# Kernel tuning notes

Hardware: AMD Instinct MI355X
Metric: run time of the kernel (lower is better)

The kernel has to match this reference:

```python
import jax, jax.numpy as jnp
import numpy as np

B, T, C = 4, 2048, 1024
H = 16
D = C // H  # head_size = 64


def setup_inputs() -> dict:
    key = jax.random.key(0)
    ks = jax.random.split(key, 9)
    s = 1.0 / np.sqrt(C).astype(np.float32)
    return {
        "x": jax.random.normal(ks[0], (B, T, C), dtype=jnp.float32),
        "Wq": jax.random.normal(ks[1], (C, C), dtype=jnp.float32) * s,
        "bq": jnp.zeros((C,), dtype=jnp.float32),
        "Wk": jax.random.normal(ks[2], (C, C), dtype=jnp.float32) * s,
        "bk": jnp.zeros((C,), dtype=jnp.float32),
        "Wv": jax.random.normal(ks[3], (C, C), dtype=jnp.float32) * s,
        "bv": jnp.zeros((C,), dtype=jnp.float32),
        "Wp": jax.random.normal(ks[4], (C, C), dtype=jnp.float32) * s,
        "bp": jnp.zeros((C,), dtype=jnp.float32),
    }


def reference(x, Wq, bq, Wk, bk, Wv, bv, Wp, bp):
    # Linear projections, then split heads: (B, T, C) -> (B, H, T, D)
    def heads(t):
        return t.reshape(B, T, H, D).transpose(0, 2, 1, 3)

    q = heads(x @ Wq + bq)
    k = heads(x @ Wk + bk)
    v = heads(x @ Wv + bv)

    scale = 1.0 / np.sqrt(D).astype(np.float32)
    att = jnp.einsum("bhqd,bhkd->bhqk", q, k) * scale  # (B, H, T, T)
    att = jax.nn.softmax(att, axis=-1)
    y = jnp.einsum("bhqk,bhkd->bhqd", att, v)  # (B, H, T, D)
    y = y.transpose(0, 2, 1, 3).reshape(B, T, C)
    return y @ Wp + bp
```

## Files before the change

kernel.cpp:

```cpp
#include <hip/hip_runtime.h>

typedef unsigned int uint;
typedef unsigned short ushort;

typedef __bf16 bf16x8 __attribute__((ext_vector_type(8)));
typedef __bf16 bf16x2 __attribute__((ext_vector_type(2)));
typedef float f32x4 __attribute__((ext_vector_type(4)));
typedef float f32x16 __attribute__((ext_vector_type(16)));
typedef uint uint2v __attribute__((ext_vector_type(2)));

union U4 { uint4 u; bf16x8 v; };
union UB2 { bf16x2 v; uint u; };

__device__ __forceinline__ ushort f2bf(float f){
  uint u = __float_as_uint(f);
  u += 0x7fffu + ((u >> 16) & 1u);
  return (ushort)(u >> 16);
}

__device__ __forceinline__ uint packbf(float lo, float hi){
  UB2 t; t.v[0] = (__bf16)lo; t.v[1] = (__bf16)hi;
  return t.u;
}

__device__ __forceinline__ float exp2a(float x){
  float r; asm("v_exp_f32 %0, %1" : "=v"(r) : "v"(x)); return r;
}

__device__ __forceinline__ void gload16(const void* g, void* l){
  __builtin_amdgcn_global_load_lds((const __attribute__((address_space(1))) uint*)g,
                                   (__attribute__((address_space(3))) uint*)l, 16, 0, 0);
}

__device__ __forceinline__ f32x16 mfma32(U4 a, U4 b, f32x16 c){
  return __builtin_amdgcn_mfma_f32_32x32x16_bf16(a.v, b.v, c, 0, 0, 0);
}

__global__ __launch_bounds__(256, 3) void gemm_qkv(
    const ushort* __restrict__ xh, const ushort* __restrict__ wbase,
    const float* __restrict__ bq, const float* __restrict__ bk,
    const float* __restrict__ bv,
    ushort* __restrict__ Qb, ushort* __restrict__ Kb, ushort* __restrict__ Vtb,
    float qscale)
{
  __shared__ uint4 smem4[2048];
  char* sAh = (char*)smem4;
  char* sBh = (char*)smem4 + 16384;

  const int tid  = threadIdx.x;
  const int lane = tid & 63;
  const int wid  = tid >> 6;
  const int wm = (wid >> 1) * 64;
  const int wn = (wid & 1) * 64;

  int hwlin = blockIdx.y * 64 + blockIdx.x;
  int xcd = hwlin & 7, io = hwlin >> 3;
  int mb  = xcd * 8 + (io & 7);
  int nv  = io >> 3;
  int nb  = nv & 7;
  int w   = nv >> 3;
  const long tm = (long)mb * 128;
  const long tn = (long)nb * 128;

  const char* gA = (const char*)xh;
  const char* gB = (const char*)(wbase + (long)w * 1048576);

  f32x4 acc[4][4] = {};

  for (int ks = 0; ks < 8; ks++){
    const int koff = ks * 128;
    #pragma unroll
    for (int c = 0; c < 4; c++){
      int o   = (tid + 256*c) * 16;
      int row = o >> 7;
      int src = (o & 127) ^ ((row & 7) << 4);
      gload16(gA + (tm + row)*2048 + koff + src, sAh + o);
      gload16(gB + (tn + row)*2048 + koff + src, sBh + o);
    }
    __syncthreads();
    #pragma unroll
    for (int k = 0; k < 2; k++){
      const int kb = k*64 + (lane >> 4)*16;
      U4 ah[4], bh[4];
      #pragma unroll
      for (int m = 0; m < 4; m++){
        int row = wm + m*16 + (lane & 15);
        ah[m].u = *(const uint4*)(sAh + row*128 + (kb ^ ((row & 7) << 4)));
      }
      #pragma unroll
      for (int n = 0; n < 4; n++){
        int row = wn + n*16 + (lane & 15);
        bh[n].u = *(const uint4*)(sBh + row*128 + (kb ^ ((row & 7) << 4)));
      }
      __builtin_amdgcn_s_setprio(1);
      #pragma unroll
      for (int m = 0; m < 4; m++)
      #pragma unroll
      for (int n = 0; n < 4; n++)
        acc[m][n] = __builtin_amdgcn_mfma_f32_16x16x32_bf16(ah[m].v, bh[n].v, acc[m][n], 0,0,0);
      __builtin_amdgcn_s_setprio(0);
    }
    __syncthreads();
  }
  for (int ks = 8; ks < 16; ks++){
    const int koff = ks * 128;
    #pragma unroll
    for (int c = 0; c < 4; c++){
      int o   = (tid + 256*c) * 16;
      int row = o >> 7;
      int src = (o & 127) ^ ((row & 7) << 4);
      gload16(gA + (tm + row)*2048 + koff + src, sAh + o);
      gload16(gB + (tn + row)*2048 + koff + src, sBh + o);
    }
    __syncthreads();
    #pragma unroll
    for (int k = 0; k < 2; k++){
      const int kb = k*64 + (lane >> 4)*16;
      U4 ah[4], bh[4];
      #pragma unroll
      for (int m = 0; m < 4; m++){
        int row = wm + m*16 + (lane & 15);
        ah[m].u = *(const uint4*)(sAh + row*128 + (kb ^ ((row & 7) << 4)));
      }
      #pragma unroll
      for (int n = 0; n < 4; n++){
        int row = wn + n*16 + (lane & 15);
        bh[n].u = *(const uint4*)(sBh + row*128 + (kb ^ ((row & 7) << 4)));
      }
      __builtin_amdgcn_s_setprio(1);
      #pragma unroll
      for (int m = 0; m < 4; m++)
      #pragma unroll
      for (int n = 0; n < 4; n++)
        acc[m][n] = __builtin_amdgcn_mfma_f32_16x16x32_bf16(ah[m].v, bh[n].v, acc[m][n], 0,0,0);
      __builtin_amdgcn_s_setprio(0);
    }
    __syncthreads();
  }

  const float* bias = (w == 0) ? bq : (w == 1) ? bk : bv;
  const float oscale = (w == 0) ? qscale : 1.0f;

  #pragma unroll
  for (int n = 0; n < 4; n++){
    int colg = (int)tn + wn + n*16 + (lane & 15);
    float bv_ = bias[colg];
    #pragma unroll
    for (int m = 0; m < 4; m++){
      int rowg0 = (int)tm + wm + m*16 + ((lane >> 4) * 4);
      float v0 = (acc[m][n][0] + bv_) * oscale;
      float v1 = (acc[m][n][1] + bv_) * oscale;
      float v2 = (acc[m][n][2] + bv_) * oscale;
      float v3 = (acc[m][n][3] + bv_) * oscale;
      if (w < 2){
        ushort* o = (w == 0) ? Qb : Kb;
        o[(long)(rowg0+0)*1024 + colg] = f2bf(v0);
        o[(long)(rowg0+1)*1024 + colg] = f2bf(v1);
        o[(long)(rowg0+2)*1024 + colg] = f2bf(v2);
        o[(long)(rowg0+3)*1024 + colg] = f2bf(v3);
      } else {
        int b = rowg0 >> 11, t0 = rowg0 & 2047;
        int h = colg >> 6, d = colg & 63;
        ushort4 o4;
        o4.x = f2bf(v0); o4.y = f2bf(v1); o4.z = f2bf(v2); o4.w = f2bf(v3);
        *(ushort4*)&Vtb[(((long)(b*16 + h))*64 + d)*2048 + t0] = o4;
      }
    }
  }
}

__global__ __launch_bounds__(256, 2) void gemm_out(
    const ushort* __restrict__ Ahp, const ushort* __restrict__ Bhp,
    const float* __restrict__ bias, float* __restrict__ outp)
{
  __shared__ uint4 smem4[2048];
  char* sAh = (char*)smem4;
  char* sBh = (char*)smem4 + 16384;

  const int tid  = threadIdx.x;
  const int lane = tid & 63;
  const int wid  = tid >> 6;
  const int wm = (wid >> 1) * 64;
  const int wn = (wid & 1) * 64;

  int lin = blockIdx.y * 64 + blockIdx.x;
  int xcd = lin & 7, j = lin >> 3;
  const long tm = (long)(xcd * 8 + (j & 7)) * 128;
  const long tn = (long)(j >> 3) * 128;

  const char* gA = (const char*)Ahp;
  const char* gB = (const char*)Bhp;

  f32x4 acc[4][4] = {};

  for (int ks = 0; ks < 16; ks++){
    const int koff = ks * 128;
    #pragma unroll
    for (int c = 0; c < 4; c++){
      int o   = (tid + 256*c) * 16;
      int row = o >> 7;
      int src = (o & 127) ^ ((row & 7) << 4);
      gload16(gA + (tm + row)*2048 + koff + src, sAh + o);
      gload16(gB + (tn + row)*2048 + koff + src, sBh + o);
    }
    __syncthreads();
    #pragma unroll
    for (int k = 0; k < 2; k++){
      const int kb = k*64 + (lane >> 4)*16;
      U4 ah[4], bh[4];
      #pragma unroll
      for (int m = 0; m < 4; m++){
        int row = wm + m*16 + (lane & 15);
        ah[m].u = *(const uint4*)(sAh + row*128 + (kb ^ ((row & 7) << 4)));
      }
      #pragma unroll
      for (int n = 0; n < 4; n++){
        int row = wn + n*16 + (lane & 15);
        bh[n].u = *(const uint4*)(sBh + row*128 + (kb ^ ((row & 7) << 4)));
      }
      __builtin_amdgcn_s_setprio(1);
      #pragma unroll
      for (int m = 0; m < 4; m++)
      #pragma unroll
      for (int n = 0; n < 4; n++)
        acc[m][n] = __builtin_amdgcn_mfma_f32_16x16x32_bf16(ah[m].v, bh[n].v, acc[m][n], 0,0,0);
      __builtin_amdgcn_s_setprio(0);
    }
    __syncthreads();
  }

  #pragma unroll
  for (int n = 0; n < 4; n++){
    int colg = (int)tn + wn + n*16 + (lane & 15);
    float bv_ = bias[colg];
    #pragma unroll
    for (int m = 0; m < 4; m++){
      int rowg0 = (int)tm + wm + m*16 + ((lane >> 4) * 4);
      #pragma unroll
      for (int r = 0; r < 4; r++)
        outp[(long)(rowg0+r)*1024 + colg] = acc[m][n][r] + bv_;
    }
  }
}

__device__ __forceinline__ void mkfrag(const uint (&pk)[8], U4 (&out)[2])
{
  #pragma unroll
  for (int kl = 0; kl < 2; kl++){
    int bb = kl*4;
    uint2v r02 = __builtin_amdgcn_permlane32_swap(pk[bb+0], pk[bb+2], false, false);
    uint2v r13 = __builtin_amdgcn_permlane32_swap(pk[bb+1], pk[bb+3], false, false);
    out[kl].u = make_uint4(r02[0], r13[0], r02[1], r13[1]);
  }
}

__global__ __launch_bounds__(128, 2) void attn_kernel(
    const ushort* __restrict__ Qg, const ushort* __restrict__ Kg,
    const ushort* __restrict__ Vtg, ushort* __restrict__ Yg)
{
  __shared__ uint4 smem[2048];
  char* sK0 = (char*)smem;
  char* sV0 = (char*)smem + 8192;
  char* sK1 = (char*)smem + 16384;
  char* sV1 = (char*)smem + 24576;

  const int tid  = threadIdx.x;
  const int lane = tid & 63;
  const int w    = tid >> 6;
  const int ql   = lane & 31;
  const int hh   = lane >> 5;

  int lin = blockIdx.y * 16 + blockIdx.x;
  int xcd = lin & 7, j = lin >> 3;
  const int bh  = (j >> 4) * 8 + xcd;
  const int qb  = j & 15;
  const int tq0 = qb * 128 + w * 64;
  const int b = bh >> 4, h = bh & 15;

  U4 qf[2][4];
  #pragma unroll
  for (int g = 0; g < 2; g++){
    const char* qrow = (const char*)Qg + (long)(b*2048 + tq0 + g*32 + ql)*2048 + h*128 + hh*16;
    #pragma unroll
    for (int c = 0; c < 4; c++) qf[g][c].u = *(const uint4*)(qrow + c*32);
  }

  f32x16 y00 = {}, y01 = {}, y10 = {}, y11 = {};
  float ls0 = 0.f, ls1 = 0.f;

  const char* kbase = (const char*)Kg  + (long)b*2048*2048 + h*128;
  const char* vbase = (const char*)Vtg + (long)bh*64*4096;

  auto stage = [&](char* dK, char* dV, int kc){
    #pragma unroll
    for (int c2 = 0; c2 < 4; c2++){
      int o   = tid*16 + c2*2048;
      int row = o >> 7;
      int src = (o & 127) ^ ((row & 7) << 4);
      gload16(kbase + (long)(kc*64 + row)*2048 + src, dK + o);
      gload16(vbase + (long)row*4096 + (long)kc*128 + src, dV + o);
    }
  };

  auto sm = [&](f32x16& s, float& ls, uint (&pk)[8]){
    float ps = 0.f;
    #pragma unroll
    for (int r = 0; r < 16; r++){ s[r] = exp2a(s[r]); ps += s[r]; }
    ls += ps;
    #pragma unroll
    for (int i = 0; i < 8; i++) pk[i] = packbf(s[2*i], s[2*i+1]);
  };

  auto body = [&](int kc, char* cK, char* cV, char* nK, char* nV){
    if (kc < 31){
      stage(nK, nV, kc + 1);
      asm volatile("s_waitcnt vmcnt(8)" ::: "memory");
    } else {
      asm volatile("s_waitcnt vmcnt(0)" ::: "memory");
    }
    __builtin_amdgcn_s_barrier();

    f32x16 s00 = {}, s10 = {};
    __builtin_amdgcn_s_setprio(1);
    #pragma unroll
    for (int ksd = 0; ksd < 4; ksd++){
      int kb = ksd*32 + hh*16;
      int r = ql;
      U4 a; a.u = *(const uint4*)(cK + r*128 + (kb ^ ((r & 7) << 4)));
      s00 = mfma32(a, qf[0][ksd], s00);
      s10 = mfma32(a, qf[1][ksd], s10);
    }
    __builtin_amdgcn_s_setprio(0);

    uint pk00[8], pk10[8];
    sm(s00, ls0, pk00); sm(s10, ls1, pk10);
    U4 f0[2], f1[2];
    mkfrag(pk00, f0); mkfrag(pk10, f1);

    f32x16 s01 = {}, s11 = {};
    __builtin_amdgcn_s_setprio(1);
    #pragma unroll
    for (int ksd = 0; ksd < 4; ksd++){
      int kb = ksd*32 + hh*16;
      int r = 32 + ql;
      U4 a; a.u = *(const uint4*)(cK + r*128 + (kb ^ ((r & 7) << 4)));
      s01 = mfma32(a, qf[0][ksd], s01);
      s11 = mfma32(a, qf[1][ksd], s11);
    }

    #pragma unroll
    for (int kl = 0; kl < 2; kl++){
      int kvo = kl*32 + hh*16;
      U4 a0, a1;
      { int r = ql;      a0.u = *(const uint4*)(cV + r*128 + (kvo ^ ((r & 7) << 4))); }
      { int r = 32 + ql; a1.u = *(const uint4*)(cV + r*128 + (kvo ^ ((r & 7) << 4))); }
      y00 = mfma32(a0, f0[kl], y00);
      y01 = mfma32(a1, f0[kl], y01);
      y10 = mfma32(a0, f1[kl], y10);
      y11 = mfma32(a1, f1[kl], y11);
    }
    __builtin_amdgcn_s_setprio(0);

    uint pk01[8], pk11[8];
    sm(s01, ls0, pk01); sm(s11, ls1, pk11);
    mkfrag(pk01, f0); mkfrag(pk11, f1);

    __builtin_amdgcn_s_setprio(1);
    #pragma unroll
    for (int kl = 0; kl < 2; kl++){
      int kvo = 64 + kl*32 + hh*16;
      U4 a0, a1;
      { int r = ql;      a0.u = *(const uint4*)(cV + r*128 + (kvo ^ ((r & 7) << 4))); }
      { int r = 32 + ql; a1.u = *(const uint4*)(cV + r*128 + (kvo ^ ((r & 7) << 4))); }
      y00 = mfma32(a0, f0[kl], y00);
      y01 = mfma32(a1, f0[kl], y01);
      y10 = mfma32(a0, f1[kl], y10);
      y11 = mfma32(a1, f1[kl], y11);
    }
    __builtin_amdgcn_s_setprio(0);

    if (kc < 31){
      asm volatile("" ::: "memory");
      __builtin_amdgcn_s_barrier();
    }
  };

  stage(sK0, sV0, 0);
  for (int kc2 = 0; kc2 < 16; kc2++){
    body(2*kc2 + 0, sK0, sV0, sK1, sV1);
    body(2*kc2 + 1, sK1, sV1, sK0, sV0);
  }

  #pragma unroll
  for (int g = 0; g < 2; g++){
    f32x16& t0 = g ? y10 : y00;
    f32x16& t1 = g ? y11 : y01;
    float ls   = g ? ls1 : ls0;
    float lt   = ls + __shfl_xor(ls, 32);
    float inv  = 1.0f / lt;
    int tq = tq0 + g*32 + ql;
    ushort* yrow = Yg + ((long)b*2048 + tq)*1024 + h*64;
    #pragma unroll
    for (int qi = 0; qi < 4; qi++){
      ushort4 o0, o1;
      o0.x = f2bf(t0[qi*4+0]*inv); o0.y = f2bf(t0[qi*4+1]*inv);
      o0.z = f2bf(t0[qi*4+2]*inv); o0.w = f2bf(t0[qi*4+3]*inv);
      o1.x = f2bf(t1[qi*4+0]*inv); o1.y = f2bf(t1[qi*4+1]*inv);
      o1.z = f2bf(t1[qi*4+2]*inv); o1.w = f2bf(t1[qi*4+3]*inv);
      *(ushort4*)(yrow + qi*8 + hh*4)      = o0;
      *(ushort4*)(yrow + 32 + qi*8 + hh*4) = o1;
    }
  }
}

__global__ void cast_x_kernel(const float* __restrict__ x, ushort* __restrict__ xh)
{
  int i = blockIdx.x*256 + threadIdx.x;
  float4 v = ((const float4*)x)[i];
  ushort4 h;
  h.x = f2bf(v.x); h.y = f2bf(v.y); h.z = f2bf(v.z); h.w = f2bf(v.w);
  ((ushort4*)xh)[i] = h;
}

__global__ void wsplit_kernel(const float* __restrict__ W0, const float* __restrict__ W1,
                              const float* __restrict__ W2, const float* __restrict__ W3,
                              ushort* __restrict__ outbase)
{
  __shared__ float tile[64][65];
  const int z = blockIdx.z;
  const float* W = (z == 0) ? W0 : (z == 1) ? W1 : (z == 2) ? W2 : W3;
  ushort* Th = outbase + (long)z * 1048576;
  const int tid = threadIdx.x;
  const int k0 = blockIdx.x * 64;
  const int n0 = blockIdx.y * 64;
  #pragma unroll
  for (int c = 0; c < 4; c++){
    int idx = tid + 256*c;
    int r = idx >> 4, c4 = idx & 15;
    float4 v = *(const float4*)&W[(long)(k0 + r)*1024 + n0 + c4*4];
    tile[r][c4*4+0] = v.x; tile[r][c4*4+1] = v.y;
    tile[r][c4*4+2] = v.z; tile[r][c4*4+3] = v.w;
  }
  __syncthreads();
  #pragma unroll
  for (int c = 0; c < 4; c++){
    int idx = tid + 256*c;
    int nr = idx >> 4, k4 = idx & 15;
    ushort4 hh;
    hh.x = f2bf(tile[k4*4+0][nr]); hh.y = f2bf(tile[k4*4+1][nr]);
    hh.z = f2bf(tile[k4*4+2][nr]); hh.w = f2bf(tile[k4*4+3][nr]);
    *(ushort4*)&Th[(long)(n0 + nr)*1024 + k0 + k4*4] = hh;
  }
}

extern "C" void kernel_launch(void* const* d_in, const int* in_sizes, int n_in,
                              void* d_out, int out_size, void* d_ws, size_t ws_size,
                              hipStream_t stream)
{
  const float* x  = (const float*)d_in[0];
  const float* Wq = (const float*)d_in[1];
  const float* bq = (const float*)d_in[2];
  const float* Wk = (const float*)d_in[3];
  const float* bk = (const float*)d_in[4];
  const float* Wv = (const float*)d_in[5];
  const float* bv = (const float*)d_in[6];
  const float* Wp = (const float*)d_in[7];
  const float* bp = (const float*)d_in[8];

  char* ws = (char*)d_ws;
  const size_t SZ_X = 16777216;
  const size_t SZ_W = 2097152;
  ushort* xh  = (ushort*)(ws);
  ushort* wqh = (ushort*)(ws + SZ_X);
  ushort* wph = (ushort*)(ws + SZ_X + 3*SZ_W);
  ushort* Qb  = (ushort*)(ws + SZ_X + 4*SZ_W);
  ushort* Kb  = (ushort*)(ws + 2*SZ_X + 4*SZ_W);
  ushort* Vtb = (ushort*)(ws + 3*SZ_X + 4*SZ_W);
  ushort* Yb  = (ushort*)(ws + 4*SZ_X + 4*SZ_W);

  cast_x_kernel<<<8192, 256, 0, stream>>>(x, xh);
  wsplit_kernel<<<dim3(16,16,4), 256, 0, stream>>>(Wq, Wk, Wv, Wp, wqh);

  gemm_qkv<<<dim3(64,24), 256, 0, stream>>>(xh, wqh, bq, bk, bv,
                                            Qb, Kb, Vtb, 0.18033688f);

  attn_kernel<<<dim3(16,64), 128, 0, stream>>>(Qb, Kb, Vtb, Yb);

  gemm_out<<<dim3(64,8), 256, 0, stream>>>(Yb, wph, bp, (float*)d_out);
}
```

Baseline: 272.6 us.

## Shrink attention and output GEMM tiles, drop attention double-buffering

Attention now gives each wave 32 query rows instead of 64, launches twice as many blocks, and replaces the double-buffered prefetch pipeline with a single-buffer load followed by syncthreads. The output GEMM uses 128x64 tiles over twice as many blocks, and the split QKV k-loop is merged into one loop. The aim is more parallelism and occupancy from smaller tiles and less shared memory. The cost is lost load/compute overlap in attention and lower K/V reuse per loaded tile, which roughly doubles K/V traffic.

New measurement: 318.5 us. +16.8%, slower.

```diff
diff --git a/kernel.cpp b/kernel.cpp
--- a/kernel.cpp
+++ b/kernel.cpp
@@ -67,42 +67,7 @@
 
   f32x4 acc[4][4] = {};
 
-  for (int ks = 0; ks < 8; ks++){
-    const int koff = ks * 128;
-    #pragma unroll
-    for (int c = 0; c < 4; c++){
-      int o   = (tid + 256*c) * 16;
-      int row = o >> 7;
-      int src = (o & 127) ^ ((row & 7) << 4);
-      gload16(gA + (tm + row)*2048 + koff + src, sAh + o);
-      gload16(gB + (tn + row)*2048 + koff + src, sBh + o);
-    }
-    __syncthreads();
-    #pragma unroll
-    for (int k = 0; k < 2; k++){
-      const int kb = k*64 + (lane >> 4)*16;
-      U4 ah[4], bh[4];
-      #pragma unroll
-      for (int m = 0; m < 4; m++){
-        int row = wm + m*16 + (lane & 15);
-        ah[m].u = *(const uint4*)(sAh + row*128 + (kb ^ ((row & 7) << 4)));
-      }
-      #pragma unroll
-      for (int n = 0; n < 4; n++){
-        int row = wn + n*16 + (lane & 15);
-        bh[n].u = *(const uint4*)(sBh + row*128 + (kb ^ ((row & 7) << 4)));
-      }
-      __builtin_amdgcn_s_setprio(1);
-      #pragma unroll
-      for (int m = 0; m < 4; m++)
-      #pragma unroll
-      for (int n = 0; n < 4; n++)
-        acc[m][n] = __builtin_amdgcn_mfma_f32_16x16x32_bf16(ah[m].v, bh[n].v, acc[m][n], 0,0,0);
-      __builtin_amdgcn_s_setprio(0);
-    }
-    __syncthreads();
-  }
-  for (int ks = 8; ks < 16; ks++){
+  for (int ks = 0; ks < 16; ks++){
     const int koff = ks * 128;
     #pragma unroll
     for (int c = 0; c < 4; c++){
@@ -169,11 +134,11 @@
   }
 }
 
-__global__ __launch_bounds__(256, 2) void gemm_out(
+__global__ __launch_bounds__(256) void gemm_out(
     const ushort* __restrict__ Ahp, const ushort* __restrict__ Bhp,
     const float* __restrict__ bias, float* __restrict__ outp)
 {
-  __shared__ uint4 smem4[2048];
+  __shared__ uint4 smem4[1536];
   char* sAh = (char*)smem4;
   char* sBh = (char*)smem4 + 16384;
 
@@ -181,17 +146,17 @@
   const int lane = tid & 63;
   const int wid  = tid >> 6;
   const int wm = (wid >> 1) * 64;
-  const int wn = (wid & 1) * 64;
+  const int wn = (wid & 1) * 32;
 
   int lin = blockIdx.y * 64 + blockIdx.x;
   int xcd = lin & 7, j = lin >> 3;
   const long tm = (long)(xcd * 8 + (j & 7)) * 128;
-  const long tn = (long)(j >> 3) * 128;
+  const long tn = (long)(j >> 3) * 64;
 
   const char* gA = (const char*)Ahp;
   const char* gB = (const char*)Bhp;
 
-  f32x4 acc[4][4] = {};
+  f32x4 acc[4][2] = {};
 
   for (int ks = 0; ks < 16; ks++){
     const int koff = ks * 128;
@@ -201,36 +166,42 @@
       int row = o >> 7;
       int src = (o & 127) ^ ((row & 7) << 4);
       gload16(gA + (tm + row)*2048 + koff + src, sAh + o);
+    }
+    #pragma unroll
+    for (int c = 0; c < 2; c++){
+      int o   = (tid + 256*c) * 16;
+      int row = o >> 7;
+      int src = (o & 127) ^ ((row & 7) << 4);
       gload16(gB + (tn + row)*2048 + koff + src, sBh + o);
     }
     __syncthreads();
     #pragma unroll
     for (int k = 0; k < 2; k++){
       const int kb = k*64 + (lane >> 4)*16;
-      U4 ah[4], bh[4];
+      U4 ah[4], bh2[2];
       #pragma unroll
       for (int m = 0; m < 4; m++){
         int row = wm + m*16 + (lane & 15);
         ah[m].u = *(const uint4*)(sAh + row*128 + (kb ^ ((row & 7) << 4)));
       }
       #pragma unroll
-      for (int n = 0; n < 4; n++){
+      for (int n = 0; n < 2; n++){
         int row = wn + n*16 + (lane & 15);
-        bh[n].u = *(const uint4*)(sBh + row*128 + (kb ^ ((row & 7) << 4)));
+        bh2[n].u = *(const uint4*)(sBh + row*128 + (kb ^ ((row & 7) << 4)));
       }
       __builtin_amdgcn_s_setprio(1);
       #pragma unroll
       for (int m = 0; m < 4; m++)
       #pragma unroll
-      for (int n = 0; n < 4; n++)
-        acc[m][n] = __builtin_amdgcn_mfma_f32_16x16x32_bf16(ah[m].v, bh[n].v, acc[m][n], 0,0,0);
+      for (int n = 0; n < 2; n++)
+        acc[m][n] = __builtin_amdgcn_mfma_f32_16x16x32_bf16(ah[m].v, bh2[n].v, acc[m][n], 0,0,0);
       __builtin_amdgcn_s_setprio(0);
     }
     __syncthreads();
   }
 
   #pragma unroll
-  for (int n = 0; n < 4; n++){
+  for (int n = 0; n < 2; n++){
     int colg = (int)tn + wn + n*16 + (lane & 15);
     float bv_ = bias[colg];
     #pragma unroll
@@ -254,15 +225,13 @@
   }
 }
 
-__global__ __launch_bounds__(128, 2) void attn_kernel(
+__global__ __launch_bounds__(128) void attn_kernel(
     const ushort* __restrict__ Qg, const ushort* __restrict__ Kg,
     const ushort* __restrict__ Vtg, ushort* __restrict__ Yg)
 {
-  __shared__ uint4 smem[2048];
-  char* sK0 = (char*)smem;
-  char* sV0 = (char*)smem + 8192;
-  char* sK1 = (char*)smem + 16384;
-  char* sV1 = (char*)smem + 24576;
+  __shared__ uint4 smem[1024];
+  char* sK = (char*)smem;
+  char* sV = (char*)smem + 8192;
 
   const int tid  = threadIdx.x;
   const int lane = tid & 63;
@@ -270,146 +239,97 @@
   const int ql   = lane & 31;
   const int hh   = lane >> 5;
 
-  int lin = blockIdx.y * 16 + blockIdx.x;
+  int lin = blockIdx.y * 32 + blockIdx.x;
   int xcd = lin & 7, j = lin >> 3;
-  const int bh  = (j >> 4) * 8 + xcd;
-  const int qb  = j & 15;
-  const int tq0 = qb * 128 + w * 64;
+  const int bh  = (j >> 5) * 8 + xcd;
+  const int qb  = j & 31;
+  const int tq0 = qb * 64 + w * 32;
   const int b = bh >> 4, h = bh & 15;
 
-  U4 qf[2][4];
-  #pragma unroll
-  for (int g = 0; g < 2; g++){
-    const char* qrow = (const char*)Qg + (long)(b*2048 + tq0 + g*32 + ql)*2048 + h*128 + hh*16;
-    #pragma unroll
-    for (int c = 0; c < 4; c++) qf[g][c].u = *(const uint4*)(qrow + c*32);
-  }
-
-  f32x16 y00 = {}, y01 = {}, y10 = {}, y11 = {};
-  float ls0 = 0.f, ls1 = 0.f;
+  U4 qf[4];
+  const char* qrow = (const char*)Qg + (long)(b*2048 + tq0 + ql)*2048 + h*128 + hh*16;
+  #pragma unroll
+  for (int c = 0; c < 4; c++) qf[c].u = *(const uint4*)(qrow + c*32);
+
+  f32x16 y0 = {}, y1 = {};
+  float ls = 0.f;
 
   const char* kbase = (const char*)Kg  + (long)b*2048*2048 + h*128;
   const char* vbase = (const char*)Vtg + (long)bh*64*4096;
 
-  auto stage = [&](char* dK, char* dV, int kc){
+  for (int kc = 0; kc < 32; kc++){
     #pragma unroll
     for (int c2 = 0; c2 < 4; c2++){
       int o   = tid*16 + c2*2048;
       int row = o >> 7;
       int src = (o & 127) ^ ((row & 7) << 4);
-      gload16(kbase + (long)(kc*64 + row)*2048 + src, dK + o);
-      gload16(vbase + (long)row*4096 + (long)kc*128 + src, dV + o);
-    }
-  };
-
-  auto sm = [&](f32x16& s, float& ls, uint (&pk)[8]){
-    float ps = 0.f;
-    #pragma unroll
-    for (int r = 0; r < 16; r++){ s[r] = exp2a(s[r]); ps += s[r]; }
-    ls += ps;
-    #pragma unroll
-    for (int i = 0; i < 8; i++) pk[i] = packbf(s[2*i], s[2*i+1]);
-  };
-
-  auto body = [&](int kc, char* cK, char* cV, char* nK, char* nV){
-    if (kc < 31){
-      stage(nK, nV, kc + 1);
-      asm volatile("s_waitcnt vmcnt(8)" ::: "memory");
-    } else {
-      asm volatile("s_waitcnt vmcnt(0)" ::: "memory");
-    }
-    __builtin_amdgcn_s_barrier();
-
-    f32x16 s00 = {}, s10 = {};
+      gload16(kbase + (long)(kc*64 + row)*2048 + src, sK + o);
+      gload16(vbase + (long)row*4096 + (long)kc*128 + src, sV + o);
+    }
+    __syncthreads();
+
+    f32x16 s0 = {}, s1 = {};
     __builtin_amdgcn_s_setprio(1);
     #pragma unroll
     for (int ksd = 0; ksd < 4; ksd++){
       int kb = ksd*32 + hh*16;
-      int r = ql;
-      U4 a; a.u = *(const uint4*)(cK + r*128 + (kb ^ ((r & 7) << 4)));
-      s00 = mfma32(a, qf[0][ksd], s00);
-      s10 = mfma32(a, qf[1][ksd], s10);
+      U4 a0, a1;
+      { int r = ql;      a0.u = *(const uint4*)(sK + r*128 + (kb ^ ((r & 7) << 4))); }
+      { int r = 32 + ql; a1.u = *(const uint4*)(sK + r*128 + (kb ^ ((r & 7) << 4))); }
+      s0 = mfma32(a0, qf[ksd], s0);
+      s1 = mfma32(a1, qf[ksd], s1);
     }
     __builtin_amdgcn_s_setprio(0);
 
-    uint pk00[8], pk10[8];
-    sm(s00, ls0, pk00); sm(s10, ls1, pk10);
+    uint pk0[8], pk1[8];
+    {
+      float ps = 0.f;
+      #pragma unroll
+      for (int r = 0; r < 16; r++){ s0[r] = exp2a(s0[r]); ps += s0[r]; }
+      #pragma unroll
+      for (int r = 0; r < 16; r++){ s1[r] = exp2a(s1[r]); ps += s1[r]; }
+      ls += ps;
+      #pragma unroll
+      for (int i = 0; i < 8; i++){
+        pk0[i] = packbf(s0[2*i], s0[2*i+1]);
+        pk1[i] = packbf(s1[2*i], s1[2*i+1]);
+      }
+    }
     U4 f0[2], f1[2];
-    mkfrag(pk00, f0); mkfrag(pk10, f1);
-
-    f32x16 s01 = {}, s11 = {};
+    mkfrag(pk0, f0); mkfrag(pk1, f1);
+
     __builtin_amdgcn_s_setprio(1);
     #pragma unroll
-    for (int ksd = 0; ksd < 4; ksd++){
-      int kb = ksd*32 + hh*16;
-      int r = 32 + ql;
-      U4 a; a.u = *(const uint4*)(cK + r*128 + (kb ^ ((r & 7) << 4)));
-      s01 = mfma32(a, qf[0][ksd], s01);
-      s11 = mfma32(a, qf[1][ksd], s11);
-    }
-
-    #pragma unroll
-    for (int kl = 0; kl < 2; kl++){
-      int kvo = kl*32 + hh*16;
-      U4 a0, a1;
-      { int r = ql;      a0.u = *(const uint4*)(cV + r*128 + (kvo ^ ((r & 7) << 4))); }
-      { int r = 32 + ql; a1.u = *(const uint4*)(cV + r*128 + (kvo ^ ((r & 7) << 4))); }
-      y00 = mfma32(a0, f0[kl], y00);
-      y01 = mfma32(a1, f0[kl], y01);
-      y10 = mfma32(a0, f1[kl], y10);
-      y11 = mfma32(a1, f1[kl], y11);
+    for (int half = 0; half < 2; half++){
+      #pragma unroll
+      for (int kl = 0; kl < 2; kl++){
+        int kvo = half*64 + kl*32 + hh*16;
+        U4 a0, a1;
+        { int r = ql;      a0.u = *(const uint4*)(sV + r*128 + (kvo ^ ((r & 7) << 4))); }
+        { int r = 32 + ql; a1.u = *(const uint4*)(sV + r*128 + (kvo ^ ((r & 7) << 4))); }
+        U4 bb = half ? f1[kl] : f0[kl];
+        y0 = mfma32(a0, bb, y0);
+        y1 = mfma32(a1, bb, y1);
+      }
     }
     __builtin_amdgcn_s_setprio(0);
 
-    uint pk01[8], pk11[8];
-    sm(s01, ls0, pk01); sm(s11, ls1, pk11);
-    mkfrag(pk01, f0); mkfrag(pk11, f1);
-
-    __builtin_amdgcn_s_setprio(1);
-    #pragma unroll
-    for (int kl = 0; kl < 2; kl++){
-      int kvo = 64 + kl*32 + hh*16;
-      U4 a0, a1;
-      { int r = ql;      a0.u = *(const uint4*)(cV + r*128 + (kvo ^ ((r & 7) << 4))); }
-      { int r = 32 + ql; a1.u = *(const uint4*)(cV + r*128 + (kvo ^ ((r & 7) << 4))); }
-      y00 = mfma32(a0, f0[kl], y00);
-      y01 = mfma32(a1, f0[kl], y01);
-      y10 = mfma32(a0, f1[kl], y10);
-      y11 = mfma32(a1, f1[kl], y11);
-    }
-    __builtin_amdgcn_s_setprio(0);
-
-    if (kc < 31){
-      asm volatile("" ::: "memory");
-      __builtin_amdgcn_s_barrier();
-    }
-  };
-
-  stage(sK0, sV0, 0);
-  for (int kc2 = 0; kc2 < 16; kc2++){
-    body(2*kc2 + 0, sK0, sV0, sK1, sV1);
-    body(2*kc2 + 1, sK1, sV1, sK0, sV0);
-  }
-
-  #pragma unroll
-  for (int g = 0; g < 2; g++){
-    f32x16& t0 = g ? y10 : y00;
-    f32x16& t1 = g ? y11 : y01;
-    float ls   = g ? ls1 : ls0;
-    float lt   = ls + __shfl_xor(ls, 32);
-    float inv  = 1.0f / lt;
-    int tq = tq0 + g*32 + ql;
-    ushort* yrow = Yg + ((long)b*2048 + tq)*1024 + h*64;
-    #pragma unroll
-    for (int qi = 0; qi < 4; qi++){
-      ushort4 o0, o1;
-      o0.x = f2bf(t0[qi*4+0]*inv); o0.y = f2bf(t0[qi*4+1]*inv);
-      o0.z = f2bf(t0[qi*4+2]*inv); o0.w = f2bf(t0[qi*4+3]*inv);
-      o1.x = f2bf(t1[qi*4+0]*inv); o1.y = f2bf(t1[qi*4+1]*inv);
-      o1.z = f2bf(t1[qi*4+2]*inv); o1.w = f2bf(t1[qi*4+3]*inv);
-      *(ushort4*)(yrow + qi*8 + hh*4)      = o0;
-      *(ushort4*)(yrow + 32 + qi*8 + hh*4) = o1;
-    }
+    __syncthreads();
+  }
+
+  float lt  = ls + __shfl_xor(ls, 32);
+  float inv = 1.0f / lt;
+  int tq = tq0 + ql;
+  ushort* yrow = Yg + ((long)b*2048 + tq)*1024 + h*64;
+  #pragma unroll
+  for (int qi = 0; qi < 4; qi++){
+    ushort4 o0, o1;
+    o0.x = f2bf(y0[qi*4+0]*inv); o0.y = f2bf(y0[qi*4+1]*inv);
+    o0.z = f2bf(y0[qi*4+2]*inv); o0.w = f2bf(y0[qi*4+3]*inv);
+    o1.x = f2bf(y1[qi*4+0]*inv); o1.y = f2bf(y1[qi*4+1]*inv);
+    o1.z = f2bf(y1[qi*4+2]*inv); o1.w = f2bf(y1[qi*4+3]*inv);
+    *(ushort4*)(yrow + qi*8 + hh*4)      = o0;
+    *(ushort4*)(yrow + 32 + qi*8 + hh*4) = o1;
   }
 }
 
@@ -484,7 +404,7 @@
   gemm_qkv<<<dim3(64,24), 256, 0, stream>>>(xh, wqh, bq, bk, bv,
                                             Qb, Kb, Vtb, 0.18033688f);
 
-  attn_kernel<<<dim3(16,64), 128, 0, stream>>>(Qb, Kb, Vtb, Yb);
-
-  gemm_out<<<dim3(64,8), 256, 0, stream>>>(Yb, wph, bp, (float*)d_out);
-}
+  attn_kernel<<<dim3(32,64), 128, 0, stream>>>(Qb, Kb, Vtb, Yb);
+
+  gemm_out<<<dim3(64,16), 256, 0, stream>>>(Yb, wph, bp, (float*)d_out);
+}
```
